# Kernel optimization log

Hardware: AMD Instinct MI355X
Metric: run time of the kernel (lower is better)

## Reference

```python
import jax, jax.numpy as jnp
import numpy as np

B, M, DM = 8, 1024, 1024
H, DH, R = 16, 64, 32
DFF, R1, R2, RO = 4096, 512, 512, 512
EPS = 1e-12


def layernorm(x, g, b):
    mu = jnp.mean(x, axis=-1, keepdims=True)
    var = jnp.mean(jnp.square(x - mu), axis=-1, keepdims=True)
    return (x - mu) * jax.lax.rsqrt(var + EPS) * g + b


def setup_inputs() -> dict:
    key = jax.random.key(0)
    ks = jax.random.split(key, 24)
    s = lambda *sh: 1.0 / np.sqrt(sh[-2] if len(sh) > 1 else sh[-1])
    d = {}
    d['x'] = jax.random.normal(ks[0], (B, M, DM), jnp.float32)
    d['mask'] = jnp.zeros((B, M), jnp.float32)  # additive attention mask
    # per-head low-rank QKV factors: P:(H,DM,R), V:(H,R,DH), b:(H,DH)
    for i, nm in enumerate(['q', 'k', 'v']):
        d['P' + nm] = jax.random.normal(ks[1 + 3 * i], (H, DM, R), jnp.float32) * 0.02
        d['V' + nm] = jax.random.normal(ks[2 + 3 * i], (H, R, DH), jnp.float32) * 0.02
        d['b' + nm] = jnp.zeros((H, DH), jnp.float32)
    # attention output projection (low-rank) + LN1
    d['Uo'] = jax.random.normal(ks[10], (DM, RO), jnp.float32) * 0.02
    d['Vo'] = jax.random.normal(ks[11], (RO, DM), jnp.float32) * 0.02
    d['bo_attn'] = jnp.zeros((DM,), jnp.float32)
    d['g1'] = jnp.ones((DM,), jnp.float32)
    d['beta1'] = jnp.zeros((DM,), jnp.float32)
    # FFN low-rank factors + LN2
    d['U1'] = jax.random.normal(ks[12], (DM, R1), jnp.float32) * 0.02
    d['V1'] = jax.random.normal(ks[13], (R1, DFF), jnp.float32) * 0.02
    d['b1'] = jnp.zeros((DFF,), jnp.float32)
    d['U2'] = jax.random.normal(ks[14], (DFF, R2), jnp.float32) * 0.02
    d['V2'] = jax.random.normal(ks[15], (R2, DM), jnp.float32) * 0.02
    d['b2'] = jnp.zeros((DM,), jnp.float32)
    d['g2'] = jnp.ones((DM,), jnp.float32)
    d['beta2'] = jnp.zeros((DM,), jnp.float32)
    return d


def reference(x, mask, Pq, Vq, bq, Pk, Vk, bk, Pv, Vv, bv,
              Uo, Vo, bo_attn, g1, beta1,
              U1, V1, b1, U2, V2, b2, g2, beta2):
    # low-rank Q/K/V: x @ P -> (B,H,M,R), then @ V -> (B,H,M,DH), + bias
    def qkv(P, V, b):
        tmp = jnp.einsum('bmd,hdr->bhmr', x, P)
        return jnp.einsum('bhmr,hre->bhme', tmp, V) + b[None, :, None, :]

    Q = qkv(Pq, Vq, bq)
    K = qkv(Pk, Vk, bk)
    V = qkv(Pv, Vv, bv)
    scale = 1.0 / jnp.sqrt(jnp.asarray(DH, x.dtype))
    scores = jnp.einsum('bhme,bhne->bhmn', Q, K) * scale
    scores = scores + mask[:, None, None, :]  # additive mask broadcast over heads/queries
    probs = jax.nn.softmax(scores, axis=-1)
    attn = jnp.einsum('bhmn,bhne->bhme', probs, V)  # (B,H,M,DH)
    attn = attn.transpose(0, 2, 1, 3).reshape(attn.shape[0], attn.shape[2], -1)  # (B,M,DM)
    x1 = layernorm(x + (attn @ Uo) @ Vo + bo_attn, g1, beta1)
    # FFN: GELU((x1 @ U1) @ V1 + b1) @ U2 @ V2 + b2 (flashsvd_ffn semantics)
    mid = x1 @ U1
    hidden = jax.nn.gelu(mid @ V1 + b1, approximate=False)
    y = (hidden @ U2) @ V2 + b2
    return layernorm(x1 + y, g2, beta2)
```

## Files before the change

### kernel.cpp

```cpp
#include <hip/hip_runtime.h>
#include <hip/hip_bf16.h>
#include <math.h>

typedef unsigned short u16;
typedef unsigned int u32;
typedef __attribute__((ext_vector_type(8))) short bf16x8;
typedef __attribute__((ext_vector_type(4))) float f32x4;
typedef __attribute__((ext_vector_type(2))) unsigned int u32x2;
typedef __attribute__((ext_vector_type(4))) unsigned int u32x4;

#define B_ 8
#define M_ 1024
#define DM_ 1024
#define H_ 16
#define DH_ 64
#define NR_ 8192

__device__ __forceinline__ u16 f2bf(float f) {
    unsigned u = __float_as_uint(f);
    u += 0x7FFFu + ((u >> 16) & 1u);
    return (u16)(u >> 16);
}

__device__ __forceinline__ float bf2f(u16 v) {
    return __uint_as_float((u32)v << 16);
}

__device__ __forceinline__ void gload16(const void* g, void* l) {
    __builtin_amdgcn_global_load_lds(
        (const __attribute__((address_space(1))) void*)g,
        (__attribute__((address_space(3))) void*)l, 16, 0, 0);
}

__device__ __forceinline__ u32 lds_addr(const void* p) {
    return (u32)(uintptr_t)(const __attribute__((address_space(3))) void*)p;
}

__device__ void conv_dev(const float* __restrict__ in, u16* __restrict__ out,
                         int bid, int tid) {
#pragma unroll
    for (int j = 0; j < 4; ++j) {
        int i = bid * 4096 + j * 1024 + tid * 4;
        float4 v = *reinterpret_cast<const float4*>(in + i);
        unsigned long long p = (unsigned long long)f2bf(v.x)
                             | ((unsigned long long)f2bf(v.y) << 16)
                             | ((unsigned long long)f2bf(v.z) << 32)
                             | ((unsigned long long)f2bf(v.w) << 48);
        *reinterpret_cast<unsigned long long*>(out + i) = p;
    }
}

__device__ void prep_p_dev(const float* __restrict__ P, u16* __restrict__ Pt,
                           int h, int kc, int tid, float* sm) {
    float (*Ps)[33] = (float(*)[33])sm;
#pragma unroll
    for (int i = 0; i < 16; ++i) {
        int e = tid + i * 256;
        int kk = e >> 5, r = e & 31;
        Ps[kk][r] = P[(size_t)h * 32768 + (size_t)(kc + kk) * 32 + r];
    }
    __syncthreads();
#pragma unroll
    for (int i = 0; i < 16; ++i) {
        int e = tid + i * 256;
        int r = e >> 7, k = e & 127;
        Pt[(size_t)(h * 32 + r) * 1024 + kc + k] = f2bf(Ps[k][r]);
    }
}

__device__ void prep_f_dev(const float* __restrict__ V, u16* __restrict__ Ft,
                           int h, int tid, float* sm) {
    float (*Vs)[65] = (float(*)[65])sm;
#pragma unroll
    for (int i = 0; i < 8; ++i) {
        int e = tid + i * 256;
        int r = e >> 6, c = e & 63;
        Vs[r][c] = V[(size_t)h * 2048 + r * 64 + c];
    }
    __syncthreads();
#pragma unroll
    for (int i = 0; i < 8; ++i) {
        int idx = tid + i * 256;
        int e = idx >> 5, r = idx & 31;
        Ft[(size_t)h * 2560 + e * 40 + r] = f2bf(Vs[r][e]);
    }
}

__device__ void transp_dev(const float* __restrict__ in, u16* __restrict__ out,
                           int R, int C, int bx, int by, int tid, float* sm) {
    float (*t)[65] = (float(*)[65])sm;
    const int rb = by * 64, cb = bx * 64;
#pragma unroll
    for (int i = 0; i < 16; ++i) {
        int e = tid + i * 256;
        int r = e >> 6, c = e & 63;
        t[r][c] = in[(size_t)(rb + r) * C + cb + c];
    }
    __syncthreads();
#pragma unroll
    for (int i = 0; i < 16; ++i) {
        int e = tid + i * 256;
        int r = e >> 6, c = e & 63;
        out[(size_t)(cb + r) * R + rb + c] = f2bf(t[c][r]);
    }
}

__global__ __launch_bounds__(256) void prep_all(
    const float* __restrict__ x,
    const float* __restrict__ Pq, const float* __restrict__ Pk, const float* __restrict__ Pv,
    const float* __restrict__ Vq, const float* __restrict__ Vk, const float* __restrict__ Vv,
    const float* __restrict__ Uo, const float* __restrict__ Vo,
    const float* __restrict__ U1, const float* __restrict__ V1,
    const float* __restrict__ U2, const float* __restrict__ V2,
    u16* __restrict__ Xb, u16* __restrict__ Pt,
    u16* __restrict__ Ftq, u16* __restrict__ Ftk, u16* __restrict__ Ftv,
    u16* __restrict__ Uot, u16* __restrict__ Vot,
    u16* __restrict__ U1t, u16* __restrict__ V1t,
    u16* __restrict__ U2t, u16* __restrict__ V2t) {
    __shared__ float smem[4224];
    const int bid = blockIdx.x, tid = threadIdx.x;
    if (bid < 2048) {
        conv_dev(x, Xb, bid, tid);
    } else if (bid < 2432) {
        int t = bid - 2048, which = t >> 7, tt = t & 127;
        const float* P = which == 0 ? Pq : (which == 1 ? Pk : Pv);
        prep_p_dev(P, Pt + (size_t)which * 524288, tt >> 3, (tt & 7) * 128, tid, smem);
    } else if (bid < 2480) {
        int t = bid - 2432, which = t >> 4;
        const float* V = which == 0 ? Vq : (which == 1 ? Vk : Vv);
        u16* F = which == 0 ? Ftq : (which == 1 ? Ftk : Ftv);
        prep_f_dev(V, F, t & 15, tid, smem);
    } else if (bid < 2608) {
        int t = bid - 2480;
        transp_dev(Uo, Uot, 1024, 512, t & 7, t >> 3, tid, smem);
    } else if (bid < 2736) {
        int t = bid - 2608;
        transp_dev(Vo, Vot, 512, 1024, t & 15, t >> 4, tid, smem);
    } else if (bid < 2864) {
        int t = bid - 2736;
        transp_dev(U1, U1t, 1024, 512, t & 7, t >> 3, tid, smem);
    } else if (bid < 3376) {
        int t = bid - 2864;
        transp_dev(V1, V1t, 512, 4096, t & 63, t >> 6, tid, smem);
    } else if (bid < 3888) {
        int t = bid - 3376;
        transp_dev(U2, U2t, 4096, 512, t & 7, t >> 3, tid, smem);
    } else {
        int t = bid - 3888;
        transp_dev(V2, V2t, 512, 1024, t & 15, t >> 4, tid, smem);
    }
}

template <int EPI, int NF>
__global__ __launch_bounds__(256) void gemm_bf16(const u16* __restrict__ A,
                                                 const u16* __restrict__ Bt,
                                                 const float* __restrict__ bias,
                                                 void* __restrict__ Cout,
                                                 int K, int N) {
    constexpr int BN = NF * 32;
    __shared__ u16 As[128 * 64];
    __shared__ u16 Bs[BN * 64];
    const int tid = threadIdx.x;
    const int lane = tid & 63, wv = tid >> 6;

    const int NX = gridDim.x;
    const int flat = blockIdx.x + blockIdx.y * NX;
    const int q = (NX * gridDim.y) >> 3;
    const int nid = (flat & 7) * q + (flat >> 3);
    const int row0 = (nid / NX) * 128, col0 = (nid % NX) * BN;

    const int frow = lane & 15, fk8 = lane >> 4;
    const int wm = (wv >> 1) * 64, wn = (wv & 1) * (BN / 2);

    f32x4 acc[4][NF];
    const f32x4 z4 = {0.f, 0.f, 0.f, 0.f};
#pragma unroll
    for (int i = 0; i < 4; ++i)
#pragma unroll
        for (int j = 0; j < NF; ++j) acc[i][j] = z4;

    for (int k0 = 0; k0 < K; k0 += 64) {
#pragma unroll
        for (int i = 0; i < 4; ++i) {
            int rr = (i * 4 + wv) * 8 + (lane >> 3);
            int cc = ((lane & 7) ^ (rr & 7)) * 8;
            gload16(A + (size_t)(row0 + rr) * K + k0 + cc,
                    (char*)As + (i * 4 + wv) * 1024);
        }
#pragma unroll
        for (int i = 0; i < NF; ++i) {
            int rr = (i * 4 + wv) * 8 + (lane >> 3);
            int cc = ((lane & 7) ^ (rr & 7)) * 8;
            gload16(Bt + (size_t)(col0 + rr) * K + k0 + cc,
                    (char*)Bs + (i * 4 + wv) * 1024);
        }
        asm volatile("s_waitcnt vmcnt(0)" ::: "memory");
        __syncthreads();
#pragma unroll
        for (int kf = 0; kf < 2; ++kf) {
            bf16x8 af[4], bfr[NF];
#pragma unroll
            for (int mf = 0; mf < 4; ++mf) {
                int r = wm + mf * 16 + frow;
                int c16 = (kf * 4 + fk8) ^ (r & 7);
                af[mf] = *reinterpret_cast<const bf16x8*>((char*)As + r * 128 + c16 * 16);
            }
#pragma unroll
            for (int nf = 0; nf < NF; ++nf) {
                int r = wn + nf * 16 + frow;
                int c16 = (kf * 4 + fk8) ^ (r & 7);
                bfr[nf] = *reinterpret_cast<const bf16x8*>((char*)Bs + r * 128 + c16 * 16);
            }
#pragma unroll
            for (int mf = 0; mf < 4; ++mf)
#pragma unroll
                for (int nf = 0; nf < NF; ++nf)
                    acc[mf][nf] = __builtin_amdgcn_mfma_f32_16x16x32_bf16(
                        af[mf], bfr[nf], acc[mf][nf], 0, 0, 0);
        }
        __syncthreads();
    }

    const int orow = fk8 * 4, ocol = frow;
#pragma unroll
    for (int mf = 0; mf < 4; ++mf)
#pragma unroll
        for (int nf = 0; nf < NF; ++nf)
#pragma unroll
            for (int j = 0; j < 4; ++j) {
                int row = row0 + wm + mf * 16 + orow + j;
                int col = col0 + wn + nf * 16 + ocol;
                float v = acc[mf][nf][j];
                if (EPI == 2) {
                    v += bias[col];
                    v = 0.5f * v * (1.f + erff(v * 0.70710678118f));
                    ((u16*)Cout)[(size_t)row * N + col] = f2bf(v);
                } else {
                    ((u16*)Cout)[(size_t)row * N + col] = f2bf(v);
                }
            }
}

__global__ __launch_bounds__(256) void gemm_qkv(const u16* __restrict__ A,
                                                const u16* __restrict__ Bt,
                                                const u16* __restrict__ Ftq,
                                                const u16* __restrict__ Ftk,
                                                const u16* __restrict__ Ftv,
                                                const float* __restrict__ bq,
                                                const float* __restrict__ bk,
                                                const float* __restrict__ bv,
                                                u16* __restrict__ Qo,
                                                u16* __restrict__ Ko,
                                                u16* __restrict__ Vo) {
    const int K = 1024;
    __shared__ u16 As[128 * 64];
    __shared__ u16 Bs[128 * 64];
    const int tid = threadIdx.x;
    const int lane = tid & 63, wv = tid >> 6;

    const int NX = gridDim.x;
    const int flat = blockIdx.x + blockIdx.y * NX;
    const int q = (NX * gridDim.y) >> 3;
    const int nid = (flat & 7) * q + (flat >> 3);
    const int row0 = (nid / NX) * 128, col0 = (nid % NX) * 128;

    const int frow = lane & 15, fk8 = lane >> 4;
    const int wm = (wv >> 1) * 64, wn = (wv & 1) * 64;

    f32x4 acc[4][4];
    const f32x4 z4 = {0.f, 0.f, 0.f, 0.f};
#pragma unroll
    for (int i = 0; i < 4; ++i)
#pragma unroll
        for (int j = 0; j < 4; ++j) acc[i][j] = z4;

    for (int k0 = 0; k0 < K; k0 += 64) {
#pragma unroll
        for (int i = 0; i < 4; ++i) {
            int rr = (i * 4 + wv) * 8 + (lane >> 3);
            int cc = ((lane & 7) ^ (rr & 7)) * 8;
            gload16(A + (size_t)(row0 + rr) * K + k0 + cc,
                    (char*)As + (i * 4 + wv) * 1024);
            gload16(Bt + (size_t)(col0 + rr) * K + k0 + cc,
                    (char*)Bs + (i * 4 + wv) * 1024);
        }
        asm volatile("s_waitcnt vmcnt(0)" ::: "memory");
        __syncthreads();
#pragma unroll
        for (int kf = 0; kf < 2; ++kf) {
            bf16x8 af[4], bfr[4];
#pragma unroll
            for (int mf = 0; mf < 4; ++mf) {
                int r = wm + mf * 16 + frow;
                int c16 = (kf * 4 + fk8) ^ (r & 7);
                af[mf] = *reinterpret_cast<const bf16x8*>((char*)As + r * 128 + c16 * 16);
            }
#pragma unroll
            for (int nf = 0; nf < 4; ++nf) {
                int r = wn + nf * 16 + frow;
                int c16 = (kf * 4 + fk8) ^ (r & 7);
                bfr[nf] = *reinterpret_cast<const bf16x8*>((char*)Bs + r * 128 + c16 * 16);
            }
#pragma unroll
            for (int mf = 0; mf < 4; ++mf)
#pragma unroll
                for (int nf = 0; nf < 4; ++nf)
                    acc[mf][nf] = __builtin_amdgcn_mfma_f32_16x16x32_bf16(
                        af[mf], bfr[nf], acc[mf][nf], 0, 0, 0);
        }
        __syncthreads();
    }

    u16* preg = (wv < 2) ? As + wv * 4096 : Bs + (wv - 2) * 4096;
#pragma unroll
    for (int mf = 0; mf < 4; ++mf)
#pragma unroll
        for (int nf = 0; nf < 4; ++nf)
#pragma unroll
            for (int j = 0; j < 4; ++j) {
                int r = mf * 16 + fk8 * 4 + j;
                int c = nf * 16 + frow;
                int byte = r * 128 + (((c >> 3) ^ (r & 7)) * 16) + (c & 7) * 2;
                *(u16*)((char*)preg + byte) = f2bf(acc[mf][nf][j]);
            }
    __syncthreads();

    const int f = col0 >> 9;
    const u16* Ft = f == 0 ? Ftq : (f == 1 ? Ftk : Ftv);
    const float* bias = f == 0 ? bq : (f == 1 ? bk : bv);
    u16* outp = f == 0 ? Qo : (f == 1 ? Ko : Vo);
    const int h0 = (((col0 & 511) + wn) >> 5);

#pragma unroll
    for (int hh = 0; hh < 2; ++hh) {
        const int h = h0 + hh;
        const u16* ftb = Ft + (size_t)h * 2560;
        bf16x8 bf2[4];
#pragma unroll
        for (int ef = 0; ef < 4; ++ef) {
            int e = ef * 16 + frow;
            bf2[ef] = *reinterpret_cast<const bf16x8*>(ftb + e * 40 + fk8 * 8);
        }
#pragma unroll
        for (int mf = 0; mf < 4; ++mf) {
            int r = mf * 16 + frow;
            bf16x8 af = *reinterpret_cast<const bf16x8*>(
                (char*)preg + r * 128 + (((hh * 4 + fk8) ^ (r & 7)) * 16));
#pragma unroll
            for (int ef = 0; ef < 4; ++ef) {
                f32x4 o = __builtin_amdgcn_mfma_f32_16x16x32_bf16(af, bf2[ef], z4, 0, 0, 0);
                int e = ef * 16 + frow;
                float bv_ = bias[h * 64 + e];
#pragma unroll
                for (int j = 0; j < 4; ++j) {
                    int row = row0 + wm + mf * 16 + fk8 * 4 + j;
                    int bb = row >> 10, m = row & 1023;
                    outp[(((size_t)(bb * 16 + h) << 10) + m) * 64 + e] = f2bf(o[j] + bv_);
                }
            }
        }
    }
}

__global__ __launch_bounds__(256) void gemm_db(const u16* __restrict__ A,
                                               const u16* __restrict__ Bt,
                                               u16* __restrict__ Cout,
                                               int K, int N) {
    __shared__ u16 As[2][128 * 64];
    __shared__ u16 Bs[2][64 * 64];
    const int tid = threadIdx.x;
    const int lane = tid & 63, wv = tid >> 6;

    const int NX = gridDim.x;
    const int flat = blockIdx.x + blockIdx.y * NX;
    const int q = (NX * gridDim.y) >> 3;
    const int nid = (flat & 7) * q + (flat >> 3);
    const int row0 = (nid / NX) * 128, col0 = (nid % NX) * 64;

    const int frow = lane & 15, fk8 = lane >> 4;
    const int wm = (wv >> 1) * 64, wn = (wv & 1) * 32;

    f32x4 acc[4][2];
    const f32x4 z4 = {0.f, 0.f, 0.f, 0.f};
#pragma unroll
    for (int i = 0; i < 4; ++i) {
        acc[i][0] = z4;
        acc[i][1] = z4;
    }

    const int srr = (lane >> 3);
    const int scc = (lane & 7);

#pragma unroll
    for (int i = 0; i < 4; ++i) {
        int rr = (i * 4 + wv) * 8 + srr;
        int cc = (scc ^ (rr & 7)) * 8;
        gload16(A + (size_t)(row0 + rr) * K + cc, (char*)&As[0][0] + (i * 4 + wv) * 1024);
    }
#pragma unroll
    for (int i = 0; i < 2; ++i) {
        int rr = (i * 4 + wv) * 8 + srr;
        int cc = (scc ^ (rr & 7)) * 8;
        gload16(Bt + (size_t)(col0 + rr) * K + cc, (char*)&Bs[0][0] + (i * 4 + wv) * 1024);
    }

    int cur = 0;
    for (int k0 = 0; k0 < K; k0 += 64) {
        __syncthreads();
        if (k0 + 64 < K) {
            int kn = k0 + 64;
#pragma unroll
            for (int i = 0; i < 4; ++i) {
                int rr = (i * 4 + wv) * 8 + srr;
                int cc = (scc ^ (rr & 7)) * 8;
                gload16(A + (size_t)(row0 + rr) * K + kn + cc,
                        (char*)&As[cur ^ 1][0] + (i * 4 + wv) * 1024);
            }
#pragma unroll
            for (int i = 0; i < 2; ++i) {
                int rr = (i * 4 + wv) * 8 + srr;
                int cc = (scc ^ (rr & 7)) * 8;
                gload16(Bt + (size_t)(col0 + rr) * K + kn + cc,
                        (char*)&Bs[cur ^ 1][0] + (i * 4 + wv) * 1024);
            }
        }
#pragma unroll
        for (int kf = 0; kf < 2; ++kf) {
            bf16x8 af[4], bfr[2];
#pragma unroll
            for (int mf = 0; mf < 4; ++mf) {
                int r = wm + mf * 16 + frow;
                int c16 = (kf * 4 + fk8) ^ (r & 7);
                af[mf] = *reinterpret_cast<const bf16x8*>((char*)&As[cur][0] + r * 128 + c16 * 16);
            }
#pragma unroll
            for (int nf = 0; nf < 2; ++nf) {
                int r = wn + nf * 16 + frow;
                int c16 = (kf * 4 + fk8) ^ (r & 7);
                bfr[nf] = *reinterpret_cast<const bf16x8*>((char*)&Bs[cur][0] + r * 128 + c16 * 16);
            }
#pragma unroll
            for (int mf = 0; mf < 4; ++mf)
#pragma unroll
                for (int nf = 0; nf < 2; ++nf)
                    acc[mf][nf] = __builtin_amdgcn_mfma_f32_16x16x32_bf16(
                        af[mf], bfr[nf], acc[mf][nf], 0, 0, 0);
        }
        cur ^= 1;
    }

#pragma unroll
    for (int mf = 0; mf < 4; ++mf)
#pragma unroll
        for (int nf = 0; nf < 2; ++nf)
#pragma unroll
            for (int j = 0; j < 4; ++j) {
                int row = row0 + wm + mf * 16 + fk8 * 4 + j;
                int col = col0 + wn + nf * 16 + frow;
                Cout[(size_t)row * N + col] = f2bf(acc[mf][nf][j]);
            }
}

__global__ __launch_bounds__(512, 8) void attn_mfma(const u16* __restrict__ Q,
                                                    const u16* __restrict__ K,
                                                    const u16* __restrict__ V,
                                                    const float* __restrict__ mask,
                                                    u16* __restrict__ O) {
    __shared__ u16 Ks[2][4096];
    __shared__ u16 Vt[16896 / 2];
    const int flat = blockIdx.x;
    const int nid = (flat & 7) * 128 + (flat >> 3);
    const int hb = nid >> 3, qt = nid & 7;
    const int b = hb >> 4, h = hb & 15;
    const int tid = threadIdx.x, lane = tid & 63, wv = tid >> 6;
    const int frow = lane & 15, fk8 = lane >> 4;
    const size_t base = (size_t)hb * 65536;
    const float LOG2E = 1.44269504089f;

    const int krr = wv * 8 + (lane >> 3);
    const int kcc = ((lane & 7) ^ (krr & 7)) * 8;

    int voff;
    {
        int r = wv;
        int keyp = (2 * (r >> 2) + (lane >> 5)) * 16 + (r & 3) * 4 + ((lane >> 1) & 3);
        int d = ((lane >> 3) & 3) * 16 + (lane & 1) * 8;
        voff = keyp * 64 + d;
    }

#pragma unroll
    for (int i = 0; i < 2; ++i) {
        int rr = (i * 8 + wv) * 8 + (lane >> 3);
        int cc = ((lane & 7) ^ (rr & 7)) * 8;
        gload16(Q + base + (size_t)(qt * 128 + rr) * 64 + cc,
                (char*)Ks + (i * 8 + wv) * 1024);
    }
    asm volatile("s_waitcnt vmcnt(0)" ::: "memory");
    __syncthreads();
    bf16x8 qfrag[2];
#pragma unroll
    for (int kf = 0; kf < 2; ++kf) {
        int qr = wv * 16 + frow;
        int c16 = (kf * 4 + fk8) ^ (qr & 7);
        qfrag[kf] = *reinterpret_cast<const bf16x8*>((char*)Ks + qr * 128 + c16 * 16);
    }
    __syncthreads();

    gload16(K + base + (size_t)krr * 64 + kcc, (char*)&Ks[0][0] + wv * 1024);
    gload16(V + base + voff, (char*)Vt + wv * 1056);
    asm volatile("s_waitcnt vmcnt(0)" ::: "memory");
    __syncthreads();

    const u32 plbase = lds_addr(Vt) + fk8 * 1056 + frow * 2;
    const float* mrow = mask + b * M_;

    float m_i = -1e30f, l_i = 0.f;
    const f32x4 z4 = {0.f, 0.f, 0.f, 0.f};
    f32x4 o_acc[4] = {z4, z4, z4, z4};

    int cur = 0;
    for (int kt = 0; kt < 16; ++kt) {
        if (kt < 15) {
            const int nxt = cur ^ 1;
            gload16(K + base + (kt + 1) * 4096 + (size_t)krr * 64 + kcc,
                    (char*)&Ks[nxt][0] + wv * 1024);
            gload16(V + base + (kt + 1) * 4096 + voff,
                    (char*)Vt + nxt * 8448 + wv * 1056);
        }

        const char* ksb = (char*)&Ks[cur][0];
        f32x4 sacc[4] = {z4, z4, z4, z4};
        __builtin_amdgcn_s_setprio(1);
#pragma unroll
        for (int kf = 0; kf < 2; ++kf)
#pragma unroll
            for (int nf = 0; nf < 4; ++nf) {
                int kr = nf * 16 + frow;
                int c16 = (kf * 4 + fk8) ^ (kr & 7);
                bf16x8 ak = *reinterpret_cast<const bf16x8*>(ksb + kr * 128 + c16 * 16);
                sacc[nf] = __builtin_amdgcn_mfma_f32_16x16x32_bf16(ak, qfrag[kf], sacc[nf], 0, 0, 0);
            }
        __builtin_amdgcn_s_setprio(0);

        float tval[4][4];
        float tmax = -1e30f;
#pragma unroll
        for (int nf = 0; nf < 4; ++nf) {
            float4 mk = *reinterpret_cast<const float4*>(mrow + kt * 64 + nf * 16 + fk8 * 4);
            float t0 = fmaf(sacc[nf][0], 0.125f, mk.x);
            float t1 = fmaf(sacc[nf][1], 0.125f, mk.y);
            float t2 = fmaf(sacc[nf][2], 0.125f, mk.z);
            float t3 = fmaf(sacc[nf][3], 0.125f, mk.w);
            tval[nf][0] = t0; tval[nf][1] = t1; tval[nf][2] = t2; tval[nf][3] = t3;
            tmax = fmaxf(tmax, fmaxf(fmaxf(t0, t1), fmaxf(t2, t3)));
        }
        tmax = fmaxf(tmax, __shfl_xor(tmax, 16));
        tmax = fmaxf(tmax, __shfl_xor(tmax, 32));

        if (__any(tmax > m_i + 8.f)) {
            float mnew = fmaxf(m_i, tmax);
            float c = exp2f((m_i - mnew) * LOG2E);
            m_i = mnew;
            l_i *= c;
#pragma unroll
            for (int j = 0; j < 4; ++j) {
                float cj = __shfl(c, fk8 * 4 + j);
#pragma unroll
                for (int nf = 0; nf < 4; ++nf) o_acc[nf][j] *= cj;
            }
        }

        const float ml = m_i * LOG2E;
        float rs = 0.f;
        u32 w0[4], w1[4];
#pragma unroll
        for (int nf = 0; nf < 4; ++nf) {
            float p0 = exp2f(fmaf(tval[nf][0], LOG2E, -ml));
            float p1 = exp2f(fmaf(tval[nf][1], LOG2E, -ml));
            float p2 = exp2f(fmaf(tval[nf][2], LOG2E, -ml));
            float p3 = exp2f(fmaf(tval[nf][3], LOG2E, -ml));
            rs += (p0 + p1) + (p2 + p3);
            w0[nf] = __builtin_amdgcn_perm(__float_as_uint(p1), __float_as_uint(p0), 0x07060302u);
            w1[nf] = __builtin_amdgcn_perm(__float_as_uint(p3), __float_as_uint(p2), 0x07060302u);
        }
        rs += __shfl_xor(rs, 16);
        rs += __shfl_xor(rs, 32);
        l_i += rs;

        const u32 vb = plbase + (u32)(cur * 8448);
#pragma unroll
        for (int kf = 0; kf < 2; ++kf) {
            u32x4 apv = {w0[kf * 2], w1[kf * 2], w0[kf * 2 + 1], w1[kf * 2 + 1]};
            bf16x8 ap;
            __builtin_memcpy(&ap, &apv, 16);
            u32 a = vb + (u32)(kf * 4224);
            u32x2 r0, r1, r2, r3, r4, r5, r6, r7;
            asm volatile("ds_read_b64_tr_b16 %0, %1" : "=&v"(r0) : "v"(a));
            asm volatile("ds_read_b64_tr_b16 %0, %1 offset:512" : "=&v"(r1) : "v"(a));
            asm volatile("ds_read_b64_tr_b16 %0, %1 offset:128" : "=&v"(r2) : "v"(a));
            asm volatile("ds_read_b64_tr_b16 %0, %1 offset:640" : "=&v"(r3) : "v"(a));
            asm volatile("ds_read_b64_tr_b16 %0, %1 offset:256" : "=&v"(r4) : "v"(a));
            asm volatile("ds_read_b64_tr_b16 %0, %1 offset:768" : "=&v"(r5) : "v"(a));
            asm volatile("ds_read_b64_tr_b16 %0, %1 offset:384" : "=&v"(r6) : "v"(a));
            asm volatile("ds_read_b64_tr_b16 %0, %1 offset:896" : "=&v"(r7) : "v"(a));
            asm volatile("s_waitcnt lgkmcnt(0)" ::: "memory");
            __builtin_amdgcn_sched_barrier(0);
            __builtin_amdgcn_s_setprio(1);
            {
                u32x4 vv = {r0.x, r0.y, r1.x, r1.y};
                bf16x8 fb; __builtin_memcpy(&fb, &vv, 16);
                o_acc[0] = __builtin_amdgcn_mfma_f32_16x16x32_bf16(ap, fb, o_acc[0], 0, 0, 0);
            }
            {
                u32x4 vv = {r2.x, r2.y, r3.x, r3.y};
                bf16x8 fb; __builtin_memcpy(&fb, &vv, 16);
                o_acc[1] = __builtin_amdgcn_mfma_f32_16x16x32_bf16(ap, fb, o_acc[1], 0, 0, 0);
            }
            {
                u32x4 vv = {r4.x, r4.y, r5.x, r5.y};
                bf16x8 fb; __builtin_memcpy(&fb, &vv, 16);
                o_acc[2] = __builtin_amdgcn_mfma_f32_16x16x32_bf16(ap, fb, o_acc[2], 0, 0, 0);
            }
            {
                u32x4 vv = {r6.x, r6.y, r7.x, r7.y};
                bf16x8 fb; __builtin_memcpy(&fb, &vv, 16);
                o_acc[3] = __builtin_amdgcn_mfma_f32_16x16x32_bf16(ap, fb, o_acc[3], 0, 0, 0);
            }
            __builtin_amdgcn_s_setprio(0);
        }

        asm volatile("s_waitcnt vmcnt(0)" ::: "memory");
        __syncthreads();
        cur ^= 1;
    }

#pragma unroll
    for (int j = 0; j < 4; ++j) {
        float lq = __shfl(l_i, fk8 * 4 + j);
        float inv = 1.f / lq;
        int grow = qt * 128 + wv * 16 + fk8 * 4 + j;
        size_t obase = ((size_t)(b * M_ + grow)) * DM_ + h * 64;
#pragma unroll
        for (int nf = 0; nf < 4; ++nf)
            O[obase + nf * 16 + frow] = f2bf(o_acc[nf][j] * inv);
    }
}

template <int MODE>
__global__ __launch_bounds__(256) void ln_bf(const u16* __restrict__ y,
                                             const float* __restrict__ resf,
                                             const u16* __restrict__ resb,
                                             const float* __restrict__ bias,
                                             const float* __restrict__ g,
                                             const float* __restrict__ beta,
                                             float* __restrict__ outf,
                                             u16* __restrict__ outb) {
    __shared__ float red[2][4];
    const int row = blockIdx.x, tid = threadIdx.x;
    const size_t base = (size_t)row * 1024 + tid * 4;

    u32x2 yp = *reinterpret_cast<const u32x2*>(y + base);
    float v0 = bf2f((u16)(yp.x & 0xFFFF)), v1 = bf2f((u16)(yp.x >> 16));
    float v2 = bf2f((u16)(yp.y & 0xFFFF)), v3 = bf2f((u16)(yp.y >> 16));

    float r0, r1, r2, r3;
    if (MODE == 0) {
        float4 r = *reinterpret_cast<const float4*>(resf + base);
        r0 = r.x; r1 = r.y; r2 = r.z; r3 = r.w;
    } else {
        u32x2 rp = *reinterpret_cast<const u32x2*>(resb + base);
        r0 = bf2f((u16)(rp.x & 0xFFFF)); r1 = bf2f((u16)(rp.x >> 16));
        r2 = bf2f((u16)(rp.y & 0xFFFF)); r3 = bf2f((u16)(rp.y >> 16));
    }
    float4 bb = *reinterpret_cast<const float4*>(bias + tid * 4);
    v0 += r0 + bb.x; v1 += r1 + bb.y; v2 += r2 + bb.z; v3 += r3 + bb.w;

    float sum = v0 + v1 + v2 + v3;
    float sq = v0 * v0 + v1 * v1 + v2 * v2 + v3 * v3;
#pragma unroll
    for (int off = 32; off; off >>= 1) {
        sum += __shfl_down(sum, off);
        sq += __shfl_down(sq, off);
    }
    if ((tid & 63) == 0) { red[0][tid >> 6] = sum; red[1][tid >> 6] = sq; }
    __syncthreads();
    sum = red[0][0] + red[0][1] + red[0][2] + red[0][3];
    sq = red[1][0] + red[1][1] + red[1][2] + red[1][3];
    float mu = sum * (1.f / 1024.f);
    float var = sq * (1.f / 1024.f) - mu * mu;
    float rstd = rsqrtf(var + 1e-12f);
    float4 gg = *reinterpret_cast<const float4*>(g + tid * 4);
    float4 be = *reinterpret_cast<const float4*>(beta + tid * 4);
    float o0 = (v0 - mu) * rstd * gg.x + be.x;
    float o1 = (v1 - mu) * rstd * gg.y + be.y;
    float o2 = (v2 - mu) * rstd * gg.z + be.z;
    float o3 = (v3 - mu) * rstd * gg.w + be.w;
    if (MODE == 1) {
        float4 o = {o0, o1, o2, o3};
        *reinterpret_cast<float4*>(outf + base) = o;
    } else {
        unsigned long long p = (unsigned long long)f2bf(o0)
                             | ((unsigned long long)f2bf(o1) << 16)
                             | ((unsigned long long)f2bf(o2) << 32)
                             | ((unsigned long long)f2bf(o3) << 48);
        *reinterpret_cast<unsigned long long*>(outb + base) = p;
    }
}

extern "C" void kernel_launch(void* const* d_in, const int* in_sizes, int n_in,
                              void* d_out, int out_size, void* d_ws, size_t ws_size,
                              hipStream_t stream) {
    const float* x    = (const float*)d_in[0];
    const float* mask = (const float*)d_in[1];
    const float* Pq   = (const float*)d_in[2];
    const float* Vq   = (const float*)d_in[3];
    const float* bq   = (const float*)d_in[4];
    const float* Pk   = (const float*)d_in[5];
    const float* Vk   = (const float*)d_in[6];
    const float* bk   = (const float*)d_in[7];
    const float* Pv   = (const float*)d_in[8];
    const float* Vv   = (const float*)d_in[9];
    const float* bv   = (const float*)d_in[10];
    const float* Uo   = (const float*)d_in[11];
    const float* Vo   = (const float*)d_in[12];
    const float* bo   = (const float*)d_in[13];
    const float* g1   = (const float*)d_in[14];
    const float* be1  = (const float*)d_in[15];
    const float* U1   = (const float*)d_in[16];
    const float* V1   = (const float*)d_in[17];
    const float* b1   = (const float*)d_in[18];
    const float* U2   = (const float*)d_in[19];
    const float* V2   = (const float*)d_in[20];
    const float* b2   = (const float*)d_in[21];
    const float* g2   = (const float*)d_in[22];
    const float* be2  = (const float*)d_in[23];
    float* out = (float*)d_out;

    const size_t MB = 1048576;
    char* ws = (char*)d_ws;
    u16* Pt  = (u16*)(ws + 0);
    u16* Ftq = (u16*)(ws + 3 * MB);
    u16* Ftk = (u16*)(ws + 3 * MB + 131072);
    u16* Ftv = (u16*)(ws + 3 * MB + 262144);
    u16* Uot = (u16*)(ws + 4 * MB);
    u16* Vot = (u16*)(ws + 5 * MB);
    u16* U1t = (u16*)(ws + 6 * MB);
    u16* V1t = (u16*)(ws + 7 * MB);
    u16* U2t = (u16*)(ws + 11 * MB);
    u16* V2t = (u16*)(ws + 15 * MB);
    u16* Xb  = (u16*)(ws + 16 * MB);
    u16* Qb  = (u16*)(ws + 56 * MB);
    u16* Kb  = (u16*)(ws + 72 * MB);
    u16* Vb  = (u16*)(ws + 88 * MB);
    u16* Ob  = (u16*)(ws + 104 * MB);
    u16* Hb  = (u16*)(ws + 32 * MB);
    u16* Yb  = (u16*)(ws + 56 * MB);
    u16* Tb  = (u16*)(ws + 96 * MB);

    prep_all<<<4016, 256, 0, stream>>>(x, Pq, Pk, Pv, Vq, Vk, Vv,
                                       Uo, Vo, U1, V1, U2, V2,
                                       Xb, Pt, Ftq, Ftk, Ftv,
                                       Uot, Vot, U1t, V1t, U2t, V2t);

    gemm_qkv<<<dim3(12, 64), 256, 0, stream>>>(Xb, Pt, Ftq, Ftk, Ftv,
                                               bq, bk, bv, Qb, Kb, Vb);

    attn_mfma<<<1024, 512, 0, stream>>>(Qb, Kb, Vb, mask, Ob);

    gemm_db<<<dim3(8, 64), 256, 0, stream>>>(Ob, Uot, Tb, 1024, 512);
    gemm_bf16<0, 4><<<dim3(8, 64), 256, 0, stream>>>(Tb, Vot, nullptr, Yb, 512, 1024);
    ln_bf<0><<<8192, 256, 0, stream>>>(Yb, x, nullptr, bo, g1, be1, nullptr, Xb);

    gemm_db<<<dim3(8, 64), 256, 0, stream>>>(Xb, U1t, Tb, 1024, 512);
    gemm_bf16<2, 4><<<dim3(32, 64), 256, 0, stream>>>(Tb, V1t, b1, Hb, 512, 4096);
    gemm_db<<<dim3(8, 64), 256, 0, stream>>>(Hb, U2t, Tb, 4096, 512);
    gemm_bf16<0, 4><<<dim3(8, 64), 256, 0, stream>>>(Tb, V2t, nullptr, Yb, 512, 1024);
    ln_bf<1><<<8192, 256, 0, stream>>>(Yb, nullptr, Xb, b2, g2, be2, out, nullptr);
}
```

Measured before the change: 339.5 us.

## Restructure attention to 64-row query tiles with single-buffered K/V and LDS-staged P

Measured after the change: 322.3 us (median of 2 runs). 5.1% less time.

```diff
diff --git a/kernel.cpp b/kernel.cpp
--- a/kernel.cpp
+++ b/kernel.cpp
@@ -461,39 +461,30 @@
             }
 }
 
-__global__ __launch_bounds__(512, 8) void attn_mfma(const u16* __restrict__ Q,
-                                                    const u16* __restrict__ K,
-                                                    const u16* __restrict__ V,
-                                                    const float* __restrict__ mask,
-                                                    u16* __restrict__ O) {
-    __shared__ u16 Ks[2][4096];
-    __shared__ u16 Vt[16896 / 2];
+__global__ __launch_bounds__(256) void attn_mfma(const u16* __restrict__ Q,
+                                                 const u16* __restrict__ K,
+                                                 const u16* __restrict__ V,
+                                                 const float* __restrict__ mask,
+                                                 u16* __restrict__ O) {
+    __shared__ u16 Ks[4096];
+    __shared__ u16 Vt[4096];
+    __shared__ u16 Pw[4096];
     const int flat = blockIdx.x;
-    const int nid = (flat & 7) * 128 + (flat >> 3);
-    const int hb = nid >> 3, qt = nid & 7;
+    const int nid = (flat & 7) * 256 + (flat >> 3);
+    const int hb = nid >> 4, qt = nid & 15;
     const int b = hb >> 4, h = hb & 15;
     const int tid = threadIdx.x, lane = tid & 63, wv = tid >> 6;
     const int frow = lane & 15, fk8 = lane >> 4;
     const size_t base = (size_t)hb * 65536;
     const float LOG2E = 1.44269504089f;
-
-    const int krr = wv * 8 + (lane >> 3);
-    const int kcc = ((lane & 7) ^ (krr & 7)) * 8;
-
-    int voff;
-    {
-        int r = wv;
-        int keyp = (2 * (r >> 2) + (lane >> 5)) * 16 + (r & 3) * 4 + ((lane >> 1) & 3);
-        int d = ((lane >> 3) & 3) * 16 + (lane & 1) * 8;
-        voff = keyp * 64 + d;
-    }
+    const int srr = lane >> 3, scc = lane & 7;
 
 #pragma unroll
     for (int i = 0; i < 2; ++i) {
-        int rr = (i * 8 + wv) * 8 + (lane >> 3);
-        int cc = ((lane & 7) ^ (rr & 7)) * 8;
-        gload16(Q + base + (size_t)(qt * 128 + rr) * 64 + cc,
-                (char*)Ks + (i * 8 + wv) * 1024);
+        int rr = (i * 4 + wv) * 8 + srr;
+        int cc = (scc ^ (rr & 7)) * 8;
+        gload16(Q + base + (size_t)(qt * 64 + rr) * 64 + cc,
+                (char*)Ks + (i * 4 + wv) * 1024);
     }
     asm volatile("s_waitcnt vmcnt(0)" ::: "memory");
     __syncthreads();
@@ -504,31 +495,45 @@
         int c16 = (kf * 4 + fk8) ^ (qr & 7);
         qfrag[kf] = *reinterpret_cast<const bf16x8*>((char*)Ks + qr * 128 + c16 * 16);
     }
-    __syncthreads();
-
-    gload16(K + base + (size_t)krr * 64 + kcc, (char*)&Ks[0][0] + wv * 1024);
-    gload16(V + base + voff, (char*)Vt + wv * 1056);
-    asm volatile("s_waitcnt vmcnt(0)" ::: "memory");
-    __syncthreads();
-
-    const u32 plbase = lds_addr(Vt) + fk8 * 1056 + frow * 2;
+
+    int voff[2];
+#pragma unroll
+    for (int i = 0; i < 2; ++i) {
+        int c = (i * 4 + wv) * 64 + lane;
+        int kb = c >> 5, db = (c >> 3) & 3, kr = (c >> 1) & 3, hf = c & 1;
+        voff[i] = (kb * 4 + kr) * 64 + db * 16 + hf * 8;
+    }
+
+    u32 vta[4];
+    {
+        u32 vt0 = lds_addr(Vt) + fk8 * 1024 + frow * 2;
+#pragma unroll
+        for (int nf = 0; nf < 4; ++nf) vta[nf] = vt0 + nf * 128;
+    }
+
+    char* pwW = (char*)Pw + wv * 2048 + frow * 128 + (fk8 & 1) * 8;
+    char* pwR = (char*)Pw + wv * 2048 + frow * 128;
     const float* mrow = mask + b * M_;
 
     float m_i = -1e30f, l_i = 0.f;
     const f32x4 z4 = {0.f, 0.f, 0.f, 0.f};
     f32x4 o_acc[4] = {z4, z4, z4, z4};
 
-    int cur = 0;
     for (int kt = 0; kt < 16; ++kt) {
-        if (kt < 15) {
-            const int nxt = cur ^ 1;
-            gload16(K + base + (kt + 1) * 4096 + (size_t)krr * 64 + kcc,
-                    (char*)&Ks[nxt][0] + wv * 1024);
-            gload16(V + base + (kt + 1) * 4096 + voff,
-                    (char*)Vt + nxt * 8448 + wv * 1056);
-        }
-
-        const char* ksb = (char*)&Ks[cur][0];
+        __syncthreads();
+#pragma unroll
+        for (int i = 0; i < 2; ++i) {
+            int rr = (i * 4 + wv) * 8 + srr;
+            int cc = (scc ^ (rr & 7)) * 8;
+            gload16(K + base + (size_t)(kt * 64 + rr) * 64 + cc,
+                    (char*)Ks + (i * 4 + wv) * 1024);
+        }
+#pragma unroll
+        for (int i = 0; i < 2; ++i)
+            gload16(V + base + kt * 4096 + voff[i], (char*)Vt + (i * 4 + wv) * 1024);
+        asm volatile("s_waitcnt vmcnt(0)" ::: "memory");
+        __syncthreads();
+
         f32x4 sacc[4] = {z4, z4, z4, z4};
         __builtin_amdgcn_s_setprio(1);
 #pragma unroll
@@ -537,7 +542,7 @@
             for (int nf = 0; nf < 4; ++nf) {
                 int kr = nf * 16 + frow;
                 int c16 = (kf * 4 + fk8) ^ (kr & 7);
-                bf16x8 ak = *reinterpret_cast<const bf16x8*>(ksb + kr * 128 + c16 * 16);
+                bf16x8 ak = *reinterpret_cast<const bf16x8*>((char*)Ks + kr * 128 + c16 * 16);
                 sacc[nf] = __builtin_amdgcn_mfma_f32_16x16x32_bf16(ak, qfrag[kf], sacc[nf], 0, 0, 0);
             }
         __builtin_amdgcn_s_setprio(0);
@@ -572,7 +577,6 @@
 
         const float ml = m_i * LOG2E;
         float rs = 0.f;
-        u32 w0[4], w1[4];
 #pragma unroll
         for (int nf = 0; nf < 4; ++nf) {
             float p0 = exp2f(fmaf(tval[nf][0], LOG2E, -ml));
@@ -580,29 +584,38 @@
             float p2 = exp2f(fmaf(tval[nf][2], LOG2E, -ml));
             float p3 = exp2f(fmaf(tval[nf][3], LOG2E, -ml));
             rs += (p0 + p1) + (p2 + p3);
-            w0[nf] = __builtin_amdgcn_perm(__float_as_uint(p1), __float_as_uint(p0), 0x07060302u);
-            w1[nf] = __builtin_amdgcn_perm(__float_as_uint(p3), __float_as_uint(p2), 0x07060302u);
+            u32 w0 = __builtin_amdgcn_perm(__float_as_uint(p1), __float_as_uint(p0), 0x07060302u);
+            u32 w1 = __builtin_amdgcn_perm(__float_as_uint(p3), __float_as_uint(p2), 0x07060302u);
+            u32x2 wp = {w0, w1};
+            *reinterpret_cast<u32x2*>(pwW + (((nf * 2 + (fk8 >> 1)) ^ (frow & 7)) * 16)) = wp;
         }
         rs += __shfl_xor(rs, 16);
         rs += __shfl_xor(rs, 32);
         l_i += rs;
 
-        const u32 vb = plbase + (u32)(cur * 8448);
 #pragma unroll
         for (int kf = 0; kf < 2; ++kf) {
-            u32x4 apv = {w0[kf * 2], w1[kf * 2], w0[kf * 2 + 1], w1[kf * 2 + 1]};
-            bf16x8 ap;
-            __builtin_memcpy(&ap, &apv, 16);
-            u32 a = vb + (u32)(kf * 4224);
+            bf16x8 ap = *reinterpret_cast<const bf16x8*>(pwR + (((kf * 4 + fk8) ^ (frow & 7)) * 16));
             u32x2 r0, r1, r2, r3, r4, r5, r6, r7;
-            asm volatile("ds_read_b64_tr_b16 %0, %1" : "=&v"(r0) : "v"(a));
-            asm volatile("ds_read_b64_tr_b16 %0, %1 offset:512" : "=&v"(r1) : "v"(a));
-            asm volatile("ds_read_b64_tr_b16 %0, %1 offset:128" : "=&v"(r2) : "v"(a));
-            asm volatile("ds_read_b64_tr_b16 %0, %1 offset:640" : "=&v"(r3) : "v"(a));
-            asm volatile("ds_read_b64_tr_b16 %0, %1 offset:256" : "=&v"(r4) : "v"(a));
-            asm volatile("ds_read_b64_tr_b16 %0, %1 offset:768" : "=&v"(r5) : "v"(a));
-            asm volatile("ds_read_b64_tr_b16 %0, %1 offset:384" : "=&v"(r6) : "v"(a));
-            asm volatile("ds_read_b64_tr_b16 %0, %1 offset:896" : "=&v"(r7) : "v"(a));
+            if (kf == 0) {
+                asm volatile("ds_read_b64_tr_b16 %0, %1" : "=&v"(r0) : "v"(vta[0]));
+                asm volatile("ds_read_b64_tr_b16 %0, %1 offset:512" : "=&v"(r1) : "v"(vta[0]));
+                asm volatile("ds_read_b64_tr_b16 %0, %1" : "=&v"(r2) : "v"(vta[1]));
+                asm volatile("ds_read_b64_tr_b16 %0, %1 offset:512" : "=&v"(r3) : "v"(vta[1]));
+                asm volatile("ds_read_b64_tr_b16 %0, %1" : "=&v"(r4) : "v"(vta[2]));
+                asm volatile("ds_read_b64_tr_b16 %0, %1 offset:512" : "=&v"(r5) : "v"(vta[2]));
+                asm volatile("ds_read_b64_tr_b16 %0, %1" : "=&v"(r6) : "v"(vta[3]));
+                asm volatile("ds_read_b64_tr_b16 %0, %1 offset:512" : "=&v"(r7) : "v"(vta[3]));
+            } else {
+                asm volatile("ds_read_b64_tr_b16 %0, %1 offset:4096" : "=&v"(r0) : "v"(vta[0]));
+                asm volatile("ds_read_b64_tr_b16 %0, %1 offset:4608" : "=&v"(r1) : "v"(vta[0]));
+                asm volatile("ds_read_b64_tr_b16 %0, %1 offset:4096" : "=&v"(r2) : "v"(vta[1]));
+                asm volatile("ds_read_b64_tr_b16 %0, %1 offset:4608" : "=&v"(r3) : "v"(vta[1]));
+                asm volatile("ds_read_b64_tr_b16 %0, %1 offset:4096" : "=&v"(r4) : "v"(vta[2]));
+                asm volatile("ds_read_b64_tr_b16 %0, %1 offset:4608" : "=&v"(r5) : "v"(vta[2]));
+                asm volatile("ds_read_b64_tr_b16 %0, %1 offset:4096" : "=&v"(r6) : "v"(vta[3]));
+                asm volatile("ds_read_b64_tr_b16 %0, %1 offset:4608" : "=&v"(r7) : "v"(vta[3]));
+            }
             asm volatile("s_waitcnt lgkmcnt(0)" ::: "memory");
             __builtin_amdgcn_sched_barrier(0);
             __builtin_amdgcn_s_setprio(1);
@@ -628,17 +641,13 @@
             }
             __builtin_amdgcn_s_setprio(0);
         }
-
-        asm volatile("s_waitcnt vmcnt(0)" ::: "memory");
-        __syncthreads();
-        cur ^= 1;
     }
 
 #pragma unroll
     for (int j = 0; j < 4; ++j) {
         float lq = __shfl(l_i, fk8 * 4 + j);
         float inv = 1.f / lq;
-        int grow = qt * 128 + wv * 16 + fk8 * 4 + j;
+        int grow = qt * 64 + wv * 16 + fk8 * 4 + j;
         size_t obase = ((size_t)(b * M_ + grow)) * DM_ + h * 64;
 #pragma unroll
         for (int nf = 0; nf < 4; ++nf)
@@ -648,7 +657,6 @@
 
 template <int MODE>
 __global__ __launch_bounds__(256) void ln_bf(const u16* __restrict__ y,
-                                             const float* __restrict__ resf,
                                              const u16* __restrict__ resb,
                                              const float* __restrict__ bias,
                                              const float* __restrict__ g,
@@ -663,15 +671,10 @@
     float v0 = bf2f((u16)(yp.x & 0xFFFF)), v1 = bf2f((u16)(yp.x >> 16));
     float v2 = bf2f((u16)(yp.y & 0xFFFF)), v3 = bf2f((u16)(yp.y >> 16));
 
-    float r0, r1, r2, r3;
-    if (MODE == 0) {
-        float4 r = *reinterpret_cast<const float4*>(resf + base);
-        r0 = r.x; r1 = r.y; r2 = r.z; r3 = r.w;
-    } else {
-        u32x2 rp = *reinterpret_cast<const u32x2*>(resb + base);
-        r0 = bf2f((u16)(rp.x & 0xFFFF)); r1 = bf2f((u16)(rp.x >> 16));
-        r2 = bf2f((u16)(rp.y & 0xFFFF)); r3 = bf2f((u16)(rp.y >> 16));
-    }
+    u32x2 rp = *reinterpret_cast<const u32x2*>(resb + base);
+    float r0 = bf2f((u16)(rp.x & 0xFFFF)), r1 = bf2f((u16)(rp.x >> 16));
+    float r2 = bf2f((u16)(rp.y & 0xFFFF)), r3 = bf2f((u16)(rp.y >> 16));
+
     float4 bb = *reinterpret_cast<const float4*>(bias + tid * 4);
     v0 += r0 + bb.x; v1 += r1 + bb.y; v2 += r2 + bb.z; v3 += r3 + bb.w;
 
@@ -765,15 +768,15 @@
     gemm_qkv<<<dim3(12, 64), 256, 0, stream>>>(Xb, Pt, Ftq, Ftk, Ftv,
                                                bq, bk, bv, Qb, Kb, Vb);
 
-    attn_mfma<<<1024, 512, 0, stream>>>(Qb, Kb, Vb, mask, Ob);
+    attn_mfma<<<2048, 256, 0, stream>>>(Qb, Kb, Vb, mask, Ob);
 
     gemm_db<<<dim3(8, 64), 256, 0, stream>>>(Ob, Uot, Tb, 1024, 512);
     gemm_bf16<0, 4><<<dim3(8, 64), 256, 0, stream>>>(Tb, Vot, nullptr, Yb, 512, 1024);
-    ln_bf<0><<<8192, 256, 0, stream>>>(Yb, x, nullptr, bo, g1, be1, nullptr, Xb);
+    ln_bf<0><<<8192, 256, 0, stream>>>(Yb, Xb, bo, g1, be1, nullptr, Xb);
 
     gemm_db<<<dim3(8, 64), 256, 0, stream>>>(Xb, U1t, Tb, 1024, 512);
     gemm_bf16<2, 4><<<dim3(32, 64), 256, 0, stream>>>(Tb, V1t, b1, Hb, 512, 4096);
     gemm_db<<<dim3(8, 64), 256, 0, stream>>>(Hb, U2t, Tb, 4096, 512);
     gemm_bf16<0, 4><<<dim3(8, 64), 256, 0, stream>>>(Tb, V2t, nullptr, Yb, 512, 1024);
-    ln_bf<1><<<8192, 256, 0, stream>>>(Yb, nullptr, Xb, b2, g2, be2, out, nullptr);
-}
+    ln_bf<1><<<8192, 256, 0, stream>>>(Yb, Xb, b2, g2, be2, out, nullptr);
+}
```
